# Kernel tuning notes

Measured on AMD Instinct MI355X. Metric: run time of the kernel, lower is better.

Reference implementation:

```python
import jax, jax.numpy as jnp
import numpy as np
from math import sqrt

D_MODEL = 1024
N_HEADS = 16
D_T = 256
D_HID = 4 * D_MODEL
EPS = 1e-6


def _rmsnorm(x):
    # RMSNorm without affine: x / sqrt(mean(x^2) + eps)
    return x * jax.lax.rsqrt(jnp.mean(x * x, axis=-1, keepdims=True) + EPS)


def setup_inputs() -> dict:
    key = jax.random.key(0)
    ks = jax.random.split(key, 16)
    s = 0.02  # weight init scale
    inp = {
        "x": jax.random.normal(ks[0], (4, 2048, D_MODEL), dtype=jnp.float32),
        "t": jax.random.normal(ks[1], (4, D_T), dtype=jnp.float32),
        # AdaRMSNorm (attn) : Linear(d_t, d_model, bias=False) weights stored (out, in)
        "attn_gamma_w": jax.random.normal(ks[2], (D_MODEL, D_T), dtype=jnp.float32) * s,
        "attn_beta_w": jax.random.normal(ks[3], (D_MODEL, D_T), dtype=jnp.float32) * s,
        # Attention projections
        "W_q": jax.random.normal(ks[4], (D_MODEL, D_MODEL), dtype=jnp.float32) * s,
        "W_k": jax.random.normal(ks[5], (D_MODEL, D_MODEL), dtype=jnp.float32) * s,
        "W_v": jax.random.normal(ks[6], (D_MODEL, D_MODEL), dtype=jnp.float32) * s,
        "W_o": jax.random.normal(ks[7], (D_MODEL, D_MODEL), dtype=jnp.float32) * s,
        "attn_alpha_w": jax.random.normal(ks[8], (D_MODEL, D_T), dtype=jnp.float32) * s,
        # AdaRMSNorm (ffn)
        "ffn_gamma_w": jax.random.normal(ks[9], (D_MODEL, D_T), dtype=jnp.float32) * s,
        "ffn_beta_w": jax.random.normal(ks[10], (D_MODEL, D_T), dtype=jnp.float32) * s,
        # SwiGLU
        "gate_w": jax.random.normal(ks[11], (D_HID, D_MODEL), dtype=jnp.float32) * s,
        "hidden_w": jax.random.normal(ks[12], (D_HID, D_MODEL), dtype=jnp.float32) * s,
        "out_w": jax.random.normal(ks[13], (D_MODEL, D_HID), dtype=jnp.float32) * s,
        "out_b": jnp.zeros((D_MODEL,), dtype=jnp.float32),
        "ffn_alpha_w": jax.random.normal(ks[14], (D_MODEL, D_T), dtype=jnp.float32) * s,
    }
    return inp


def _ada_rmsnorm(x, t, gamma_w, beta_w):
    gamma = (t @ gamma_w.T)[:, None, :]  # [b, 1, d]
    beta = (t @ beta_w.T)[:, None, :]
    return gamma * _rmsnorm(x) + beta


def _attention(x, W_q, W_k, W_v, W_o):
    b, l, dm = x.shape
    d_head = dm // N_HEADS
    scale = sqrt(N_HEADS / dm)  # == 1/sqrt(d_head)
    def split(y):  # [b, l, dm] -> [b, n, l, d]
        return y.reshape(b, l, N_HEADS, d_head).transpose(0, 2, 1, 3)
    q = split(x @ W_q.T)
    k = split(x @ W_k.T)
    v = split(x @ W_v.T)
    attn = jax.nn.softmax(scale * jnp.einsum("bnqd,bnkd->bnqk", q, k), axis=-1)
    o = jnp.einsum("bnqk,bnkd->bnqd", attn, v)
    o = o.transpose(0, 2, 1, 3).reshape(b, l, dm)
    return o @ W_o.T


def _swiglu(x, gate_w, hidden_w, out_w, out_b):
    return (jax.nn.silu(x @ gate_w.T) * (x @ hidden_w.T)) @ out_w.T + out_b


def reference(x, t, attn_gamma_w, attn_beta_w, W_q, W_k, W_v, W_o, attn_alpha_w,
              ffn_gamma_w, ffn_beta_w, gate_w, hidden_w, out_w, out_b, ffn_alpha_w):
    a_alpha = (t @ attn_alpha_w.T)[:, None, :]
    x = x + a_alpha * _attention(_ada_rmsnorm(x, t, attn_gamma_w, attn_beta_w), W_q, W_k, W_v, W_o)
    f_alpha = (t @ ffn_alpha_w.T)[:, None, :]
    return x + f_alpha * _swiglu(_ada_rmsnorm(x, t, ffn_gamma_w, ffn_beta_w), gate_w, hidden_w, out_w, out_b)
```

## Files before the change

### kernel.cpp

```cpp
#include <hip/hip_runtime.h>
#include <hip/hip_bf16.h>

typedef __attribute__((ext_vector_type(8))) short short8;
typedef __attribute__((ext_vector_type(4))) short short4v;
typedef __attribute__((ext_vector_type(4))) float f32x4;
using bf16 = __hip_bfloat16;

#define BARF()  asm volatile("s_barrier" ::: "memory")
#define LGKM0() asm volatile("s_waitcnt lgkmcnt(0)" ::: "memory")
#define VMC4()  asm volatile("s_waitcnt vmcnt(4)" ::: "memory")
#define VMC0()  asm volatile("s_waitcnt vmcnt(0)" ::: "memory")
#define PRIO1() __builtin_amdgcn_s_setprio(1)
#define PRIO0() __builtin_amdgcn_s_setprio(0)

static __device__ __forceinline__ short bfb(float f) {
  bf16 h = __float2bfloat16(f);
  short r; __builtin_memcpy(&r, &h, 2); return r;
}

static __device__ __forceinline__ void gld_lds16(const bf16* g, bf16* l) {
  __builtin_amdgcn_global_load_lds(
      (const __attribute__((address_space(1))) void*)g,
      (__attribute__((address_space(3))) void*)l, 16, 0, 0);
}

__global__ __launch_bounds__(256) void cvt_all_kernel(
    const float* __restrict__ s0, const float* __restrict__ s1, const float* __restrict__ s2,
    const float* __restrict__ s3, const float* __restrict__ gw, const float* __restrict__ hw,
    const float* __restrict__ ow, bf16* __restrict__ dbase) {
  size_t c = (size_t)blockIdx.x * 256 + threadIdx.x;
  const float* src; size_t se;
  if (c < 524288) {
    int seg = (int)(c >> 17);
    src = (seg == 0) ? s0 : (seg == 1) ? s1 : (seg == 2) ? s2 : s3;
    se = (c - ((size_t)seg << 17)) * 8;
  } else if (c < 1572864) {
    size_t lc = c - 524288;
    size_t row = lc >> 7;
    src = (row & 1) ? hw : gw;
    se = ((row >> 1) << 10) + ((lc & 127) << 3);
  } else { src = ow; se = (c - 1572864) * 8; }
  float4 v0 = *(const float4*)(src + se);
  float4 v1 = *(const float4*)(src + se + 4);
  short8 o;
  o[0] = bfb(v0.x); o[1] = bfb(v0.y); o[2] = bfb(v0.z); o[3] = bfb(v0.w);
  o[4] = bfb(v1.x); o[5] = bfb(v1.y); o[6] = bfb(v1.z); o[7] = bfb(v1.w);
  *(short8*)(dbase + c * 8) = o;
}

__global__ __launch_bounds__(256) void tproj_kernel(const float* __restrict__ t,
    const float* __restrict__ w0, const float* __restrict__ w1, const float* __restrict__ w2,
    const float* __restrict__ w3, const float* __restrict__ w4, const float* __restrict__ w5,
    float* __restrict__ out) {
  int gid = blockIdx.x * 256 + threadIdx.x;
  int s = gid >> 12, rem = gid & 4095;
  int b = rem >> 10, n = rem & 1023;
  const float* w = (s == 0) ? w0 : (s == 1) ? w1 : (s == 2) ? w2 : (s == 3) ? w3 : (s == 4) ? w4 : w5;
  const float4* tv = (const float4*)(t + b * 256);
  const float4* wv = (const float4*)(w + n * 256);
  float acc = 0.f;
  #pragma unroll 8
  for (int j = 0; j < 64; ++j) {
    float4 a = tv[j], c = wv[j];
    acc += a.x * c.x + a.y * c.y + a.z * c.z + a.w * c.w;
  }
  out[gid] = acc;
}

__global__ __launch_bounds__(256) void ada_rms_kernel(const float* __restrict__ x,
    const float* __restrict__ gamma, const float* __restrict__ beta, bf16* __restrict__ out) {
  int row = blockIdx.x;
  int b = row >> 11;
  int tid = threadIdx.x;
  const float* xr = x + (size_t)row * 1024;
  float4 v = *(const float4*)(xr + tid * 4);
  float ss = v.x * v.x + v.y * v.y + v.z * v.z + v.w * v.w;
  #pragma unroll
  for (int m = 1; m < 64; m <<= 1) ss += __shfl_xor(ss, m);
  __shared__ float red[4];
  if ((tid & 63) == 0) red[tid >> 6] = ss;
  __syncthreads();
  float tot = red[0] + red[1] + red[2] + red[3];
  float rinv = rsqrtf(tot * (1.0f / 1024.0f) + 1e-6f);
  const float* g  = gamma + b * 1024 + tid * 4;
  const float* be = beta  + b * 1024 + tid * 4;
  short4v o;
  o[0] = bfb(g[0] * v.x * rinv + be[0]);
  o[1] = bfb(g[1] * v.y * rinv + be[1]);
  o[2] = bfb(g[2] * v.z * rinv + be[2]);
  o[3] = bfb(g[3] * v.w * rinv + be[3]);
  *(short4v*)(out + (size_t)row * 1024 + tid * 4) = o;
}

enum { EPI8_QKV = 0, EPI8_GH = 1 };

template<int EPI>
__global__ __launch_bounds__(512, 2) void gemm8p_kernel(
    const bf16* __restrict__ A, const bf16* __restrict__ B,
    int N, int K,
    bf16* __restrict__ o1, bf16* __restrict__ o2, bf16* __restrict__ o3)
{
  __shared__ __align__(16) bf16 sA[2 * 2 * 128 * 64];
  __shared__ __align__(16) bf16 sB[2 * 2 * 128 * 64];
  const int tid = threadIdx.x;
  const int lane = tid & 63, w = tid >> 6;
  const int wr = w >> 2, wcn = w & 3;
  const int ntn = N >> 8;
  const int trow = (int)(blockIdx.x / ntn) << 8;
  const int tcol = (int)(blockIdx.x % ntn) << 8;
  const int fr = lane & 15, hi = lane >> 4;
  const int rbase = hi << 2;
  const int NITER = K >> 7;
  const int st_row = (w << 4) + (lane >> 3);
  const int st_col = (((lane & 7) ^ ((lane >> 3) & 7)) << 3);
  const bf16* AsH0 = A + (size_t)(trow + st_row) * K + st_col;
  const bf16* AsH1 = AsH0 + (size_t)128 * K;
  const bf16* BsH0 = B + (size_t)(tcol + st_row) * K + st_col;
  const bf16* BsH1 = BsH0 + (size_t)128 * K;
  const size_t K8 = (size_t)K << 3;
  bf16* dA = sA + (w << 10);
  bf16* dB = sB + (w << 10);

  auto stA = [&](int dbuf, int h, int t) {
    const bf16* s = (h ? AsH1 : AsH0) + (t << 6);
    bf16* d = dA + ((dbuf * 2 + h) << 13);
    gld_lds16(s, d);
    gld_lds16(s + K8, d + 512);
  };
  auto stB = [&](int dbuf, int h, int t) {
    const bf16* s = (h ? BsH1 : BsH0) + (t << 6);
    bf16* d = dB + ((dbuf * 2 + h) << 13);
    gld_lds16(s, d);
    gld_lds16(s + K8, d + 512);
  };
  const int colK0 = (hi << 3) ^ ((fr & 7) << 3);
  const int colK1 = (32 + (hi << 3)) ^ ((fr & 7) << 3);
  const bf16* aB[2] = { sA + (wr << 13) + (fr << 6) + colK0,
                        sA + (wr << 13) + (fr << 6) + colK1 };
  const bf16* bB[2] = { sB + ((wcn >> 1) << 13) + ((wcn & 1) << 12) + (fr << 6) + colK0,
                        sB + ((wcn >> 1) << 13) + ((wcn & 1) << 12) + (fr << 6) + colK1 };

  f32x4 acc[8][4] = {};
  short8 a[4][2], b0[2][2], b1[2][2];

  auto RDA = [&](int dbuf, int mh) {
    #pragma unroll
    for (int mq = 0; mq < 4; ++mq)
      #pragma unroll
      for (int kk = 0; kk < 2; ++kk)
        a[mq][kk] = *(const short8*)(aB[kk] + dbuf * 16384 + (mh * 4 + mq) * 1024);
  };
  auto RDB0 = [&](int dbuf, int nh) {
    #pragma unroll
    for (int nq = 0; nq < 2; ++nq)
      #pragma unroll
      for (int kk = 0; kk < 2; ++kk)
        b0[nq][kk] = *(const short8*)(bB[kk] + dbuf * 16384 + (nh * 2 + nq) * 1024);
  };
  auto RDB1 = [&](int dbuf, int nh) {
    #pragma unroll
    for (int nq = 0; nq < 2; ++nq)
      #pragma unroll
      for (int kk = 0; kk < 2; ++kk)
        b1[nq][kk] = *(const short8*)(bB[kk] + dbuf * 16384 + (nh * 2 + nq) * 1024);
  };
  auto QUAD0 = [&](int mh, int nh) {
    #pragma unroll
    for (int mq = 0; mq < 4; ++mq)
      #pragma unroll
      for (int nq = 0; nq < 2; ++nq)
        #pragma unroll
        for (int kk = 0; kk < 2; ++kk)
          acc[mh * 4 + mq][nh * 2 + nq] = __builtin_amdgcn_mfma_f32_16x16x32_bf16(
              a[mq][kk], b0[nq][kk], acc[mh * 4 + mq][nh * 2 + nq], 0, 0, 0);
  };
  auto QUAD1 = [&](int mh, int nh) {
    #pragma unroll
    for (int mq = 0; mq < 4; ++mq)
      #pragma unroll
      for (int nq = 0; nq < 2; ++nq)
        #pragma unroll
        for (int kk = 0; kk < 2; ++kk)
          acc[mh * 4 + mq][nh * 2 + nq] = __builtin_amdgcn_mfma_f32_16x16x32_bf16(
              a[mq][kk], b1[nq][kk], acc[mh * 4 + mq][nh * 2 + nq], 0, 0, 0);
  };

  stB(0, 0, 0); stB(0, 1, 0); stA(0, 0, 0); stA(0, 1, 0);
  stB(1, 0, 1); stB(1, 1, 1);
  VMC4();
  BARF();

  for (int i = 0; i < NITER; ++i) {
    const int t1 = 2 * i + 1, tn0 = 2 * i + 2, tn1 = 2 * i + 3;
    const bool g = (i != NITER - 1);
    RDA(0, 0); RDB0(0, 0);
    stA(1, 0, t1);
    BARF(); LGKM0(); PRIO1(); QUAD0(0, 0); PRIO0(); BARF();
    RDB1(0, 1);
    stA(1, 1, t1);
    BARF(); LGKM0(); PRIO1(); QUAD1(0, 1); PRIO0(); BARF();
    RDA(0, 1);
    if (g) stB(0, 0, tn0);
    BARF(); LGKM0(); PRIO1(); QUAD1(1, 1); PRIO0(); BARF();
    if (g) stB(0, 1, tn0);
    BARF(); LGKM0(); PRIO1(); QUAD0(1, 0); PRIO0();
    if (g) { VMC4(); } else { VMC0(); }
    BARF();
    RDA(1, 0); RDB0(1, 0);
    if (g) stA(0, 0, tn0);
    BARF(); LGKM0(); PRIO1(); QUAD0(0, 0); PRIO0(); BARF();
    RDB1(1, 1);
    if (g) stA(0, 1, tn0);
    BARF(); LGKM0(); PRIO1(); QUAD1(0, 1); PRIO0(); BARF();
    RDA(1, 1);
    if (g) stB(1, 0, tn1);
    BARF(); LGKM0(); PRIO1(); QUAD1(1, 1); PRIO0(); BARF();
    if (g) stB(1, 1, tn1);
    BARF(); LGKM0(); PRIO1(); QUAD0(1, 0); PRIO0();
    if (g) { VMC4(); }
    BARF();
  }

  #pragma unroll
  for (int m = 0; m < 8; ++m)
  #pragma unroll
  for (int n = 0; n < 4; ++n)
  #pragma unroll
  for (int r = 0; r < 4; ++r) {
    int row = trow + (wr << 7) + m * 16 + rbase + r;
    int col = tcol + (wcn << 6) + n * 16 + fr;
    float c = acc[m][n][r];
    if constexpr (EPI == EPI8_QKV) {
      int seg = col >> 10, cc = col & 1023;
      int b = row >> 11, l = row & 2047, h = cc >> 6, dd = cc & 63;
      if (seg == 0)      o1[(((size_t)(b * 16 + h) * 2048 + l) << 6) + dd] = __float2bfloat16(c);
      else if (seg == 1) o2[(((size_t)(b * 16 + h) * 2048 + l) << 6) + dd] = __float2bfloat16(c);
      else               o3[(((size_t)(b * 16 + h) * 64 + dd) << 11) + l] = __float2bfloat16(c);
    } else {
      float other = __shfl_xor(c, 1);
      if (!(fr & 1)) {
        float sg = c / (1.f + __expf(-c));
        o1[(size_t)row * 4096 + (col >> 1)] = __float2bfloat16(sg * other);
      }
    }
  }
}

enum { EPI_RESID = 0, EPI_FINAL = 1 };

template<int EPI>
__global__ __launch_bounds__(256) void gemm_bt_kernel(
    const bf16* __restrict__ A, const bf16* __restrict__ B,
    int N, int K,
    float* __restrict__ outF,
    const float* __restrict__ aux1, const float* __restrict__ aux2,
    const float* __restrict__ bias)
{
  __shared__ __align__(16) bf16 As[128][32];
  __shared__ __align__(16) bf16 Bs[128][32];
  const int tid = threadIdx.x;
  const int lane = tid & 63, wid = tid >> 6;
  const int wr = wid >> 1, wc = wid & 1;
  const int ntn = N >> 7;
  const int trow = (int)(blockIdx.x / ntn) << 7;
  const int tcol = (int)(blockIdx.x % ntn) << 7;
  const int fr = lane & 15, fc = (lane >> 4) << 3;
  const int rbase = (lane >> 4) << 2;
  const bf16* gA0 = A + (size_t)(trow + wid * 32 + (lane >> 2)) * K + ((lane & 3) << 3);
  const bf16* gA1 = gA0 + (size_t)16 * K;
  const bf16* gB0 = B + (size_t)(tcol + wid * 32 + (lane >> 2)) * K + ((lane & 3) << 3);
  const bf16* gB1 = gB0 + (size_t)16 * K;
  bf16* lA0 = &As[wid * 32][0];
  bf16* lA1 = &As[wid * 32 + 16][0];
  bf16* lB0 = &Bs[wid * 32][0];
  bf16* lB1 = &Bs[wid * 32 + 16][0];
  f32x4 acc[4][4] = {};
  for (int k0 = 0; k0 < K; k0 += 32) {
    __syncthreads();
    gld_lds16(gA0 + k0, lA0);
    gld_lds16(gA1 + k0, lA1);
    gld_lds16(gB0 + k0, lB0);
    gld_lds16(gB1 + k0, lB1);
    __syncthreads();
    short8 af[4], bfr[4];
    #pragma unroll
    for (int m = 0; m < 4; ++m) af[m] = *(const short8*)&As[wr * 64 + m * 16 + fr][fc];
    #pragma unroll
    for (int n = 0; n < 4; ++n) bfr[n] = *(const short8*)&Bs[wc * 64 + n * 16 + fr][fc];
    #pragma unroll
    for (int m = 0; m < 4; ++m)
      #pragma unroll
      for (int n = 0; n < 4; ++n)
        acc[m][n] = __builtin_amdgcn_mfma_f32_16x16x32_bf16(af[m], bfr[n], acc[m][n], 0, 0, 0);
  }
  #pragma unroll
  for (int m = 0; m < 4; ++m)
  #pragma unroll
  for (int n = 0; n < 4; ++n)
  #pragma unroll
  for (int r = 0; r < 4; ++r) {
    int row = trow + wr * 64 + m * 16 + rbase + r;
    int col = tcol + wc * 64 + n * 16 + fr;
    float c = acc[m][n][r];
    int b = row >> 11;
    size_t idx = (size_t)row * 1024 + col;
    if constexpr (EPI == EPI_RESID) {
      outF[idx] = aux1[idx] + aux2[b * 1024 + col] * c;
    } else {
      outF[idx] = aux1[idx] + aux2[b * 1024 + col] * (c + bias[col]);
    }
  }
}

__global__ __launch_bounds__(256) void attn_kernel(const bf16* __restrict__ q,
    const bf16* __restrict__ k, const bf16* __restrict__ vt, bf16* __restrict__ o) {
  const int id = blockIdx.x;
  const int bh = (id & 7) * 8 + ((id >> 3) >> 4);
  const int qt = (id >> 3) & 15;
  const int b = bh >> 4, h = bh & 15;
  __shared__ __align__(16) bf16 Ks[64][72];
  __shared__ __align__(16) bf16 Vs[64][72];
  __shared__ __align__(16) bf16 Ps[128][72];
  const int tid = threadIdx.x, lane = tid & 63, w = tid >> 6;
  const int fr = lane & 15, hi = lane >> 4;
  const int fc = hi << 3, rbase = hi << 2;
  const bf16* qbase = q + ((size_t)bh * 2048 + qt * 128) * 64;
  const bf16* kbase = k + (size_t)bh * 2048 * 64;
  const bf16* vbase = vt + (size_t)bh * 64 * 2048;
  short8 qf[2][2];
  #pragma unroll
  for (int nq = 0; nq < 2; ++nq)
    #pragma unroll
    for (int ks = 0; ks < 2; ++ks)
      qf[nq][ks] = *(const short8*)(qbase + (size_t)(w * 32 + nq * 16 + fr) * 64 + ks * 32 + fc);
  f32x4 accO[4][2] = {};
  float den[2] = {};
  const float cf = 0.125f * 1.44269504089f;
  const int sr = tid >> 3, sc = (tid & 7) << 3;
  short8 rk0 = *(const short8*)(kbase + (size_t)sr * 64 + sc);
  short8 rk1 = *(const short8*)(kbase + (size_t)(sr + 32) * 64 + sc);
  short8 rv0 = *(const short8*)(vbase + (size_t)sr * 2048 + sc);
  short8 rv1 = *(const short8*)(vbase + (size_t)(sr + 32) * 2048 + sc);
  for (int kt = 0; kt < 2048; kt += 64) {
    __syncthreads();
    *(short8*)&Ks[sr][sc]      = rk0;
    *(short8*)&Ks[sr + 32][sc] = rk1;
    *(short8*)&Vs[sr][sc]      = rv0;
    *(short8*)&Vs[sr + 32][sc] = rv1;
    __syncthreads();
    if (kt + 64 < 2048) {
      rk0 = *(const short8*)(kbase + (size_t)(kt + 64 + sr) * 64 + sc);
      rk1 = *(const short8*)(kbase + (size_t)(kt + 96 + sr) * 64 + sc);
      rv0 = *(const short8*)(vbase + (size_t)sr * 2048 + kt + 64 + sc);
      rv1 = *(const short8*)(vbase + (size_t)(sr + 32) * 2048 + kt + 64 + sc);
    }
    f32x4 s[4][2] = {};
    #pragma unroll
    for (int ks = 0; ks < 2; ++ks) {
      short8 kf[4];
      #pragma unroll
      for (int mk = 0; mk < 4; ++mk) kf[mk] = *(const short8*)&Ks[mk * 16 + fr][ks * 32 + fc];
      #pragma unroll
      for (int mk = 0; mk < 4; ++mk)
        #pragma unroll
        for (int nq = 0; nq < 2; ++nq)
          s[mk][nq] = __builtin_amdgcn_mfma_f32_16x16x32_bf16(kf[mk], qf[nq][ks], s[mk][nq], 0, 0, 0);
    }
    #pragma unroll
    for (int mk = 0; mk < 4; ++mk)
      #pragma unroll
      for (int nq = 0; nq < 2; ++nq) {
        short4v pk;
        float d0 = exp2f(cf * s[mk][nq][0]);
        float d1 = exp2f(cf * s[mk][nq][1]);
        float d2 = exp2f(cf * s[mk][nq][2]);
        float d3 = exp2f(cf * s[mk][nq][3]);
        pk[0] = bfb(d0); pk[1] = bfb(d1); pk[2] = bfb(d2); pk[3] = bfb(d3);
        den[nq] += (d0 + d1) + (d2 + d3);
        *(short4v*)&Ps[w * 32 + nq * 16 + fr][mk * 16 + rbase] = pk;
      }
    __syncthreads();
    #pragma unroll
    for (int ks2 = 0; ks2 < 2; ++ks2) {
      short8 av[4], bp[2];
      #pragma unroll
      for (int nd = 0; nd < 4; ++nd) av[nd] = *(const short8*)&Vs[nd * 16 + fr][ks2 * 32 + fc];
      #pragma unroll
      for (int nq = 0; nq < 2; ++nq) bp[nq] = *(const short8*)&Ps[w * 32 + nq * 16 + fr][ks2 * 32 + fc];
      #pragma unroll
      for (int nd = 0; nd < 4; ++nd)
        #pragma unroll
        for (int nq = 0; nq < 2; ++nq)
          accO[nd][nq] = __builtin_amdgcn_mfma_f32_16x16x32_bf16(av[nd], bp[nq], accO[nd][nq], 0, 0, 0);
    }
  }
  float rd[2];
  #pragma unroll
  for (int nq = 0; nq < 2; ++nq) {
    float d = den[nq];
    d += __shfl_xor(d, 16);
    d += __shfl_xor(d, 32);
    rd[nq] = 1.0f / d;
  }
  #pragma unroll
  for (int nd = 0; nd < 4; ++nd)
    #pragma unroll
    for (int nq = 0; nq < 2; ++nq) {
      short4v ov;
      #pragma unroll
      for (int r = 0; r < 4; ++r) ov[r] = bfb(accO[nd][nq][r] * rd[nq]);
      int qrow = qt * 128 + w * 32 + nq * 16 + fr;
      int col = h * 64 + nd * 16 + rbase;
      *(short4v*)&o[((size_t)b * 2048 + qrow) * 1024 + col] = ov;
    }
}

extern "C" void kernel_launch(void* const* d_in, const int* in_sizes, int n_in,
                              void* d_out, int out_size, void* d_ws, size_t ws_size,
                              hipStream_t stream) {
  (void)in_sizes; (void)n_in; (void)out_size; (void)ws_size;
  const float* x   = (const float*)d_in[0];
  const float* t   = (const float*)d_in[1];
  const float* agw = (const float*)d_in[2];
  const float* abw = (const float*)d_in[3];
  const float* wq  = (const float*)d_in[4];
  const float* wk  = (const float*)d_in[5];
  const float* wv  = (const float*)d_in[6];
  const float* wo  = (const float*)d_in[7];
  const float* aaw = (const float*)d_in[8];
  const float* fgw = (const float*)d_in[9];
  const float* fbw = (const float*)d_in[10];
  const float* gw  = (const float*)d_in[11];
  const float* hw  = (const float*)d_in[12];
  const float* ow  = (const float*)d_in[13];
  const float* ob  = (const float*)d_in[14];
  const float* faw = (const float*)d_in[15];
  float* out = (float*)d_out;

  char* p = (char*)d_ws;
  auto alloc = [&](size_t bytes) -> char* {
    char* r = p; p += (bytes + 255) & ~(size_t)255; return r;
  };
  float* tp    = (float*)alloc((size_t)6 * 4096 * 4);
  bf16* wq_b   = (bf16*)alloc((size_t)1024 * 1024 * 2);
  bf16* wk_b   = (bf16*)alloc((size_t)1024 * 1024 * 2);
  bf16* wv_b   = (bf16*)alloc((size_t)1024 * 1024 * 2);
  bf16* wo_b   = (bf16*)alloc((size_t)1024 * 1024 * 2);
  bf16* wgh_b  = (bf16*)alloc((size_t)8192 * 1024 * 2);
  bf16* wout_b = (bf16*)alloc((size_t)1024 * 4096 * 2);
  bf16* xn_b   = (bf16*)alloc((size_t)8192 * 1024 * 2);
  bf16* q_b    = (bf16*)alloc((size_t)8192 * 1024 * 2);
  bf16* k_b    = (bf16*)alloc((size_t)8192 * 1024 * 2);
  bf16* vt_b   = (bf16*)alloc((size_t)8192 * 1024 * 2);
  bf16* ao_b   = (bf16*)alloc((size_t)8192 * 1024 * 2);
  float* xmid  = (float*)alloc((size_t)8192 * 1024 * 4);
  bf16* gh_b   = (bf16*)alloc((size_t)8192 * 4096 * 2);

  cvt_all_kernel<<<8192, 256, 0, stream>>>(wq, wk, wv, wo, gw, hw, ow, wq_b);
  tproj_kernel<<<96, 256, 0, stream>>>(t, agw, abw, aaw, fgw, fbw, faw, tp);
  ada_rms_kernel<<<8192, 256, 0, stream>>>(x, tp + 0 * 4096, tp + 1 * 4096, xn_b);
  gemm8p_kernel<EPI8_QKV><<<384, 512, 0, stream>>>(xn_b, wq_b, 3072, 1024, q_b, k_b, vt_b);
  attn_kernel<<<1024, 256, 0, stream>>>(q_b, k_b, vt_b, ao_b);
  gemm_bt_kernel<EPI_RESID><<<512, 256, 0, stream>>>(ao_b, wo_b, 1024, 1024, xmid, x, tp + 2 * 4096, nullptr);
  ada_rms_kernel<<<8192, 256, 0, stream>>>(xmid, tp + 3 * 4096, tp + 4 * 4096, xn_b);
  gemm8p_kernel<EPI8_GH><<<1024, 512, 0, stream>>>(xn_b, wgh_b, 8192, 1024, gh_b, nullptr, nullptr);
  gemm_bt_kernel<EPI_FINAL><<<512, 256, 0, stream>>>(gh_b, wout_b, 1024, 4096, out, xmid, tp + 5 * 4096, ob);
}
```

Before: 602.7 us.

## Fold softmax scale into Q, compute denominator via MFMA with ones, reorder MFMA loops

The QKV epilogue now multiplies Q by scale*log2(e), so the attention kernel applies exp2 directly without a per-element multiply. The softmax denominator is computed by an extra MFMA of a ones vector against the bf16 P tile, replacing the VALU accumulation and the cross-lane shuffle reduction. The GEMM's MFMA inner loops are reordered so kk is outermost. The denominator now sums bf16-rounded P values, which matches the numerator's rounding but adds MFMA work.

```diff
diff --git a/kernel.cpp b/kernel.cpp
--- a/kernel.cpp
+++ b/kernel.cpp
@@ -166,21 +166,21 @@
   };
   auto QUAD0 = [&](int mh, int nh) {
     #pragma unroll
-    for (int mq = 0; mq < 4; ++mq)
-      #pragma unroll
-      for (int nq = 0; nq < 2; ++nq)
+    for (int kk = 0; kk < 2; ++kk)
+      #pragma unroll
+      for (int mq = 0; mq < 4; ++mq)
         #pragma unroll
-        for (int kk = 0; kk < 2; ++kk)
+        for (int nq = 0; nq < 2; ++nq)
           acc[mh * 4 + mq][nh * 2 + nq] = __builtin_amdgcn_mfma_f32_16x16x32_bf16(
               a[mq][kk], b0[nq][kk], acc[mh * 4 + mq][nh * 2 + nq], 0, 0, 0);
   };
   auto QUAD1 = [&](int mh, int nh) {
     #pragma unroll
-    for (int mq = 0; mq < 4; ++mq)
-      #pragma unroll
-      for (int nq = 0; nq < 2; ++nq)
+    for (int kk = 0; kk < 2; ++kk)
+      #pragma unroll
+      for (int mq = 0; mq < 4; ++mq)
         #pragma unroll
-        for (int kk = 0; kk < 2; ++kk)
+        for (int nq = 0; nq < 2; ++nq)
           acc[mh * 4 + mq][nh * 2 + nq] = __builtin_amdgcn_mfma_f32_16x16x32_bf16(
               a[mq][kk], b1[nq][kk], acc[mh * 4 + mq][nh * 2 + nq], 0, 0, 0);
   };
@@ -233,8 +233,9 @@
     if constexpr (EPI == EPI8_QKV) {
       int seg = col >> 10, cc = col & 1023;
       int b = row >> 11, l = row & 2047, h = cc >> 6, dd = cc & 63;
-      if (seg == 0)      o1[(((size_t)(b * 16 + h) * 2048 + l) << 6) + dd] = __float2bfloat16(c);
-      else if (seg == 1) o2[(((size_t)(b * 16 + h) * 2048 + l) << 6) + dd] = __float2bfloat16(c);
+      if (seg == 0) {
+        o1[(((size_t)(b * 16 + h) * 2048 + l) << 6) + dd] = __float2bfloat16(c * 0.18033688f);
+      } else if (seg == 1) o2[(((size_t)(b * 16 + h) * 2048 + l) << 6) + dd] = __float2bfloat16(c);
       else               o3[(((size_t)(b * 16 + h) * 64 + dd) << 11) + l] = __float2bfloat16(c);
     } else {
       float other = __shfl_xor(c, 1);
@@ -333,9 +334,11 @@
     #pragma unroll
     for (int ks = 0; ks < 2; ++ks)
       qf[nq][ks] = *(const short8*)(qbase + (size_t)(w * 32 + nq * 16 + fr) * 64 + ks * 32 + fc);
+  short8 onesf;
+  #pragma unroll
+  for (int j = 0; j < 8; ++j) onesf[j] = (short)0x3F80;
   f32x4 accO[4][2] = {};
-  float den[2] = {};
-  const float cf = 0.125f * 1.44269504089f;
+  f32x4 accD[2] = {};
   const int sr = tid >> 3, sc = (tid & 7) << 3;
   short8 rk0 = *(const short8*)(kbase + (size_t)sr * 64 + sc);
   short8 rk1 = *(const short8*)(kbase + (size_t)(sr + 32) * 64 + sc);
@@ -371,12 +374,10 @@
       #pragma unroll
       for (int nq = 0; nq < 2; ++nq) {
         short4v pk;
-        float d0 = exp2f(cf * s[mk][nq][0]);
-        float d1 = exp2f(cf * s[mk][nq][1]);
-        float d2 = exp2f(cf * s[mk][nq][2]);
-        float d3 = exp2f(cf * s[mk][nq][3]);
-        pk[0] = bfb(d0); pk[1] = bfb(d1); pk[2] = bfb(d2); pk[3] = bfb(d3);
-        den[nq] += (d0 + d1) + (d2 + d3);
+        pk[0] = bfb(exp2f(s[mk][nq][0]));
+        pk[1] = bfb(exp2f(s[mk][nq][1]));
+        pk[2] = bfb(exp2f(s[mk][nq][2]));
+        pk[3] = bfb(exp2f(s[mk][nq][3]));
         *(short4v*)&Ps[w * 32 + nq * 16 + fr][mk * 16 + rbase] = pk;
       }
     __syncthreads();
@@ -392,16 +393,14 @@
         #pragma unroll
         for (int nq = 0; nq < 2; ++nq)
           accO[nd][nq] = __builtin_amdgcn_mfma_f32_16x16x32_bf16(av[nd], bp[nq], accO[nd][nq], 0, 0, 0);
+      #pragma unroll
+      for (int nq = 0; nq < 2; ++nq)
+        accD[nq] = __builtin_amdgcn_mfma_f32_16x16x32_bf16(onesf, bp[nq], accD[nq], 0, 0, 0);
     }
   }
   float rd[2];
   #pragma unroll
-  for (int nq = 0; nq < 2; ++nq) {
-    float d = den[nq];
-    d += __shfl_xor(d, 16);
-    d += __shfl_xor(d, 32);
-    rd[nq] = 1.0f / d;
-  }
+  for (int nq = 0; nq < 2; ++nq) rd[nq] = 1.0f / accD[nq][0];
   #pragma unroll
   for (int nd = 0; nd < 4; ++nd)
     #pragma unroll
```

New measurement: 581.2 us. -3.6%, faster.
